# Kernel optimization log

Measured on AMD Instinct MI355X. Metric: run time of the kernel, lower is better.

Reference implementation:

```python
import jax, jax.numpy as jnp
import numpy as np

FSIZE = 5
PAD = FSIZE // 2


def _conv(mosaick, filts):
    # mosaick [B,1,H,W], filts [f,f,K] -> responses [B,K,H,W].
    # Cross-correlation with edge-clamped boundary (Halide clamp semantics).
    x = jnp.pad(mosaick, ((0, 0), (0, 0), (PAD, PAD), (PAD, PAD)), mode='edge')
    k = jnp.transpose(filts, (2, 0, 1))[:, None, :, :]  # [K,1,f,f] OIHW
    return jax.lax.conv_general_dilated(
        x, k, window_strides=(1, 1), padding='VALID',
        dimension_numbers=('NCHW', 'OIHW', 'NCHW'))


def setup_inputs() -> dict:
    key = jax.random.key(0)
    k1, k2, k3 = jax.random.split(key, 3)
    B, H, W, K, f = 16, 512, 512, 8, FSIZE
    std = 1.0 / (f * f)  # matches normal_(0, 1/(fsize*fsize))
    return {
        'mosaick': jax.random.normal(k1, (B, 1, H, W), dtype=jnp.float32),
        'sel_filts': jax.random.normal(k2, (f, f, K), dtype=jnp.float32) * std,
        'green_filts': jax.random.normal(k3, (f, f, K), dtype=jnp.float32) * std,
    }


def reference(mosaick, sel_filts, green_filts):
    # Per-pixel soft filter selection over K candidate green-interpolation filters.
    sel = _conv(mosaick, sel_filts)      # [B,K,H,W] selection scores
    grn = _conv(mosaick, green_filts)    # [B,K,H,W] candidate green estimates
    w = jax.nn.softmax(sel, axis=1)      # softmax over filter bank
    interp = jnp.sum(w * grn, axis=1, keepdims=True)  # [B,1,H,W]
    # GRBG Bayer: green where row parity == col parity; copy known greens.
    H, W = mosaick.shape[-2], mosaick.shape[-1]
    yy = jnp.arange(H)[:, None]
    xx = jnp.arange(W)[None, :]
    is_green = (yy % 2) == (xx % 2)      # [H,W] bool
    # Output green channel only (module returns output[:, 1:2, ...]).
    return jnp.where(is_green, mosaick, interp)
```

## Files before the change

### kernel.cpp

```cpp
#include <hip/hip_runtime.h>


typedef float f32x16 __attribute__((ext_vector_type(16)));
typedef short s16x8  __attribute__((ext_vector_type(8)));

#define HH 512
#define WW 512
#define TW 64
#define TH 16
#define RS 80
#define NROW 20
#define NEL 72

__device__ __forceinline__ unsigned short bf16rne(float x) {
    unsigned u = __float_as_uint(x);
    u += 0x7fffu + ((u >> 16) & 1u);
    return (unsigned short)(u >> 16);
}
__device__ __forceinline__ int pk2(float hi, float lo) {
    return (int)((((unsigned)bf16rne(hi)) << 16) | (unsigned)bf16rne(lo));
}
__device__ __forceinline__ float hi16(int v) { return __uint_as_float(((unsigned)v) & 0xffff0000u); }
__device__ __forceinline__ float lo16(int v) { return __uint_as_float(((unsigned)v) << 16); }

__global__ void build_frags_kernel(const float* __restrict__ sf,
                                   const float* __restrict__ gf,
                                   short* __restrict__ ws)
{
    const int lane = threadIdx.x;
    const int mm   = lane & 31;
    const int h    = (lane >> 5) & 1;
    const int c    = mm >> 1;
    const bool tg  = mm & 1;
    const bool chok = mm < 16;
    const float* fb = tg ? gf : sf;

    s16x8 A[6];
#pragma unroll
    for (int f = 0; f < 6; ++f)
#pragma unroll
        for (int j = 0; j < 8; ++j) A[f][j] = 0;

#pragma unroll
    for (int j = 0; j < 8; ++j) {
        const int dx0 = j - 1;
        if (dx0 >= 0 && dx0 < 5 && chok) {
            A[0][j] = (short)bf16rne(fb[((h)     * 5 + dx0) * 8 + c]);
            A[1][j] = (short)bf16rne(fb[((2 + h) * 5 + dx0) * 8 + c]);
            if (h == 0)
                A[2][j] = (short)bf16rne(fb[(4 * 5 + dx0) * 8 + c]);
        }
        const int dx1 = j;
        if (dx1 < 5 && chok) {
            if (h == 1)
                A[3][j] = (short)bf16rne(fb[(0 * 5 + dx1) * 8 + c]);
            A[4][j] = (short)bf16rne(fb[((1 + h) * 5 + dx1) * 8 + c]);
            A[5][j] = (short)bf16rne(fb[((3 + h) * 5 + dx1) * 8 + c]);
        }
    }
    s16x8* dst = (s16x8*)(ws + lane * 48);
#pragma unroll
    for (int f = 0; f < 6; ++f) dst[f] = A[f];
}

__global__ __launch_bounds__(256) void demosaick_kernel(
    const float* __restrict__ mos,
    const short* __restrict__ frg,
    float* __restrict__ out)
{
    __shared__ alignas(16) unsigned short tileS[NROW * RS];

    const int tid   = threadIdx.x;
    const int bx    = blockIdx.x;
    const int by    = blockIdx.y;
    const int bimg  = blockIdx.z;
    const int tileX = bx * TW;
    const int tileY = by * TH;
    const float* img = mos + (size_t)bimg * HH * WW;

    const bool interior = (bx >= 1) && (bx <= 6) && (by >= 1) && (by <= 30);
    if (interior) {
        if (tid < 180) {
            int r = tid / 9, s = tid - 9 * r;
            const float2* src = (const float2*)(img + (size_t)(tileY - 2 + r) * WW
                                                + (tileX - 2 + 8 * s));
            float2 v0 = src[0], v1 = src[1], v2 = src[2], v3 = src[3];
            int4 d;
            d.x = pk2(v0.y, v0.x);
            d.y = pk2(v1.y, v1.x);
            d.z = pk2(v2.y, v2.x);
            d.w = pk2(v3.y, v3.x);
            *(int4*)&tileS[r * RS + 8 * s] = d;
        }
    } else {
        for (int i = tid; i < NROW * NEL; i += 256) {
            int r = i / NEL, e = i - NEL * r;
            int gy = min(max(tileY - 2 + r, 0), HH - 1);
            int gx = min(max(tileX - 2 + e, 0), WW - 1);
            tileS[r * RS + e] = bf16rne(img[(size_t)gy * WW + gx]);
        }
    }

    const int lane = tid & 63;
    const int w    = tid >> 6;
    const int n    = lane & 31;
    const int h    = lane >> 5;

    const s16x8* wsf = (const s16x8*)(frg + lane * 48);
    const s16x8 Aa0 = wsf[0], Ab0 = wsf[1], Ac0 = wsf[2];
    const s16x8 Aa1 = wsf[3], Ab1 = wsf[4], Ac1 = wsf[5];

    __syncthreads();

    const int* tb = (const int*)tileS;
    float* outp = out + (size_t)bimg * HH * WW;

#pragma unroll
    for (int pp = 0; pp < 2; ++pp) {
        const int Rl = 4 * w + 2 * pp;
        const int y  = tileY + Rl;
        const int ia = (Rl + h) * 40 + n;

        union { int4 v; s16x8 s; } Ba, Bb, Bc;
        Ba.v.x = tb[ia];       Ba.v.y = tb[ia + 1];
        Ba.v.z = tb[ia + 2];   Ba.v.w = tb[ia + 3];
        Bb.v.x = tb[ia + 80];  Bb.v.y = tb[ia + 81];
        Bb.v.z = tb[ia + 82];  Bb.v.w = tb[ia + 83];
        Bc.v.x = tb[ia + 160]; Bc.v.y = tb[ia + 161];
        Bc.v.z = tb[ia + 162]; Bc.v.w = tb[ia + 163];

        f32x16 acc = (f32x16)(0.f);
        acc = __builtin_amdgcn_mfma_f32_32x32x16_bf16(Aa0, Ba.s, acc, 0, 0, 0);
        acc = __builtin_amdgcn_mfma_f32_32x32x16_bf16(Ab0, Bb.s, acc, 0, 0, 0);
        acc = __builtin_amdgcn_mfma_f32_32x32x16_bf16(Ac0, Bc.s, acc, 0, 0, 0);
        {
            float den = 0.f, num = 0.f;
#pragma unroll
            for (int j = 0; j < 4; ++j) {
                float e = __expf(acc[2 * j]);
                den += e;
                num = fmaf(e, acc[2 * j + 1], num);
            }
            int nd  = pk2(num, den);
            int nd2 = __shfl_xor(nd, 32);
            num += hi16(nd2);
            den += lo16(nd2);
            const float interp = num * __builtin_amdgcn_rcpf(den);
            if (h == 0) {
                const int x0 = tileX + 2 * n;
                const float green = img[(size_t)y * WW + x0];
                float2 st; st.x = green; st.y = interp;
                *(float2*)(outp + (size_t)y * WW + x0) = st;
            }
        }

        f32x16 acc2 = (f32x16)(0.f);
        acc2 = __builtin_amdgcn_mfma_f32_32x32x16_bf16(Aa1, Ba.s, acc2, 0, 0, 0);
        acc2 = __builtin_amdgcn_mfma_f32_32x32x16_bf16(Ab1, Bb.s, acc2, 0, 0, 0);
        acc2 = __builtin_amdgcn_mfma_f32_32x32x16_bf16(Ac1, Bc.s, acc2, 0, 0, 0);
        {
            float den = 0.f, num = 0.f;
#pragma unroll
            for (int j = 0; j < 4; ++j) {
                float e = __expf(acc2[2 * j]);
                den += e;
                num = fmaf(e, acc2[2 * j + 1], num);
            }
            int nd  = pk2(num, den);
            int nd2 = __shfl_xor(nd, 32);
            num += hi16(nd2);
            den += lo16(nd2);
            const float interp = num * __builtin_amdgcn_rcpf(den);
            if (h == 0) {
                const int x0 = tileX + 2 * n;
                const float green = img[(size_t)(y + 1) * WW + x0 + 1];
                float2 st; st.x = interp; st.y = green;
                *(float2*)(outp + (size_t)(y + 1) * WW + x0) = st;
            }
        }
    }
}

extern "C" void kernel_launch(void* const* d_in, const int* in_sizes, int n_in,
                              void* d_out, int out_size, void* d_ws, size_t ws_size,
                              hipStream_t stream) {
    const float* mos = (const float*)d_in[0];
    const float* sf  = (const float*)d_in[1];
    const float* gf  = (const float*)d_in[2];
    float* out = (float*)d_out;
    short* ws  = (short*)d_ws;

    const int B = in_sizes[0] / (HH * WW);

    build_frags_kernel<<<1, 64, 0, stream>>>(sf, gf, ws);

    dim3 grid(WW / TW, HH / TH, B);
    dim3 block(256);
    demosaick_kernel<<<grid, block, 0, stream>>>(mos, (const short*)ws, out);
}
```

Measured before the change: 85.73 us.

## Fuse fragment build into main kernel and merge even/odd MFMA passes

Removes the separate fragment-building launch, so each block now builds its bf16 filter fragments directly from the filter arrays in registers. The A-matrix layout is reorganised so a single 3-MFMA chain produces both even- and odd-row results (rows 0-15 and 16-31 of the output tile), halving MFMA count per row pair. B fragments for four tile rows are loaded once and shared across the two passes. The edge-clamp path is unified into the vectorised loader with a per-chunk clamped fallback. In exchange, every block redoes the filter gathers and bf16 conversion.

Result: no change. 84.45 us (-1.5%).

```diff
diff --git a/kernel.cpp b/kernel.cpp
--- a/kernel.cpp
+++ b/kernel.cpp
@@ -10,7 +10,6 @@
 #define TH 16
 #define RS 80
 #define NROW 20
-#define NEL 72
 
 __device__ __forceinline__ unsigned short bf16rne(float x) {
     unsigned u = __float_as_uint(x);
@@ -23,160 +22,123 @@
 __device__ __forceinline__ float hi16(int v) { return __uint_as_float(((unsigned)v) & 0xffff0000u); }
 __device__ __forceinline__ float lo16(int v) { return __uint_as_float(((unsigned)v) << 16); }
 
-__global__ void build_frags_kernel(const float* __restrict__ sf,
-                                   const float* __restrict__ gf,
-                                   short* __restrict__ ws)
-{
-    const int lane = threadIdx.x;
-    const int mm   = lane & 31;
-    const int h    = (lane >> 5) & 1;
-    const int c    = mm >> 1;
-    const bool tg  = mm & 1;
-    const bool chok = mm < 16;
-    const float* fb = tg ? gf : sf;
-
-    s16x8 A[6];
-#pragma unroll
-    for (int f = 0; f < 6; ++f)
-#pragma unroll
-        for (int j = 0; j < 8; ++j) A[f][j] = 0;
-
-#pragma unroll
-    for (int j = 0; j < 8; ++j) {
-        const int dx0 = j - 1;
-        if (dx0 >= 0 && dx0 < 5 && chok) {
-            A[0][j] = (short)bf16rne(fb[((h)     * 5 + dx0) * 8 + c]);
-            A[1][j] = (short)bf16rne(fb[((2 + h) * 5 + dx0) * 8 + c]);
-            if (h == 0)
-                A[2][j] = (short)bf16rne(fb[(4 * 5 + dx0) * 8 + c]);
-        }
-        const int dx1 = j;
-        if (dx1 < 5 && chok) {
-            if (h == 1)
-                A[3][j] = (short)bf16rne(fb[(0 * 5 + dx1) * 8 + c]);
-            A[4][j] = (short)bf16rne(fb[((1 + h) * 5 + dx1) * 8 + c]);
-            A[5][j] = (short)bf16rne(fb[((3 + h) * 5 + dx1) * 8 + c]);
-        }
-    }
-    s16x8* dst = (s16x8*)(ws + lane * 48);
-#pragma unroll
-    for (int f = 0; f < 6; ++f) dst[f] = A[f];
-}
-
 __global__ __launch_bounds__(256) void demosaick_kernel(
     const float* __restrict__ mos,
-    const short* __restrict__ frg,
+    const float* __restrict__ sf,
+    const float* __restrict__ gf,
     float* __restrict__ out)
 {
     __shared__ alignas(16) unsigned short tileS[NROW * RS];
 
     const int tid   = threadIdx.x;
-    const int bx    = blockIdx.x;
-    const int by    = blockIdx.y;
-    const int bimg  = blockIdx.z;
-    const int tileX = bx * TW;
-    const int tileY = by * TH;
-    const float* img = mos + (size_t)bimg * HH * WW;
+    const int tileX = blockIdx.x * TW;
+    const int tileY = blockIdx.y * TH;
+    const float* img = mos + (size_t)blockIdx.z * HH * WW;
 
-    const bool interior = (bx >= 1) && (bx <= 6) && (by >= 1) && (by <= 30);
-    if (interior) {
-        if (tid < 180) {
-            int r = tid / 9, s = tid - 9 * r;
-            const float2* src = (const float2*)(img + (size_t)(tileY - 2 + r) * WW
-                                                + (tileX - 2 + 8 * s));
+    if (tid < 180) {
+        int r = tid / 9, s = tid - 9 * r;
+        int gy = min(max(tileY - 2 + r, 0), HH - 1);
+        const float* rowp = img + (size_t)gy * WW;
+        int cx = tileX - 2 + 8 * s;
+        int4 d;
+        if (cx >= 0 && cx + 8 <= WW) {
+            const float2* src = (const float2*)(rowp + cx);
             float2 v0 = src[0], v1 = src[1], v2 = src[2], v3 = src[3];
-            int4 d;
             d.x = pk2(v0.y, v0.x);
             d.y = pk2(v1.y, v1.x);
             d.z = pk2(v2.y, v2.x);
             d.w = pk2(v3.y, v3.x);
-            *(int4*)&tileS[r * RS + 8 * s] = d;
+        } else {
+            float v[8];
+#pragma unroll
+            for (int j = 0; j < 8; ++j)
+                v[j] = rowp[min(max(cx + j, 0), WW - 1)];
+            d.x = pk2(v[1], v[0]);
+            d.y = pk2(v[3], v[2]);
+            d.z = pk2(v[5], v[4]);
+            d.w = pk2(v[7], v[6]);
         }
-    } else {
-        for (int i = tid; i < NROW * NEL; i += 256) {
-            int r = i / NEL, e = i - NEL * r;
-            int gy = min(max(tileY - 2 + r, 0), HH - 1);
-            int gx = min(max(tileX - 2 + e, 0), WW - 1);
-            tileS[r * RS + e] = bf16rne(img[(size_t)gy * WW + gx]);
+        *(int4*)&tileS[r * RS + 8 * s] = d;
+    }
+
+    const int lane = tid & 63;
+    const int m    = lane & 31;
+    const int h    = lane >> 5;
+    const int mc   = m & 15;
+    const int c    = mc >> 1;
+    const float* fb = (mc & 1) ? gf : sf;
+
+    s16x8 A0 = {0, 0, 0, 0, 0, 0, 0, 0}, A1 = A0, A2 = A0;
+#pragma unroll
+    for (int j = 0; j < 8; ++j) {
+        if (m < 16) {
+            int dx = j - 1;
+            if (dx >= 0 && dx < 5) {
+                A0[j] = (short)bf16rne(fb[(h * 5 + dx) * 8 + c]);
+                A1[j] = (short)bf16rne(fb[((2 + h) * 5 + dx) * 8 + c]);
+                if (h == 0)
+                    A2[j] = (short)bf16rne(fb[(20 + dx) * 8 + c]);
+            }
+        } else {
+            if (j < 5) {
+                if (h == 1)
+                    A0[j] = (short)bf16rne(fb[j * 8 + c]);
+                A1[j] = (short)bf16rne(fb[((1 + h) * 5 + j) * 8 + c]);
+                A2[j] = (short)bf16rne(fb[((3 + h) * 5 + j) * 8 + c]);
+            }
         }
     }
 
-    const int lane = tid & 63;
-    const int w    = tid >> 6;
-    const int n    = lane & 31;
-    const int h    = lane >> 5;
-
-    const s16x8* wsf = (const s16x8*)(frg + lane * 48);
-    const s16x8 Aa0 = wsf[0], Ab0 = wsf[1], Ac0 = wsf[2];
-    const s16x8 Aa1 = wsf[3], Ab1 = wsf[4], Ac1 = wsf[5];
-
     __syncthreads();
 
+    const int w = tid >> 6;
+    const int n = lane & 31;
     const int* tb = (const int*)tileS;
-    float* outp = out + (size_t)bimg * HH * WW;
+    float* outp = out + (size_t)blockIdx.z * HH * WW;
+
+    union { int4 v; s16x8 s; } F0, F1, F2, F3;
+    {
+        const int i0 = (4 * w + h) * 40 + n;
+        F0.v.x = tb[i0];       F0.v.y = tb[i0 + 1];   F0.v.z = tb[i0 + 2];   F0.v.w = tb[i0 + 3];
+        F1.v.x = tb[i0 + 80];  F1.v.y = tb[i0 + 81];  F1.v.z = tb[i0 + 82];  F1.v.w = tb[i0 + 83];
+        F2.v.x = tb[i0 + 160]; F2.v.y = tb[i0 + 161]; F2.v.z = tb[i0 + 162]; F2.v.w = tb[i0 + 163];
+        F3.v.x = tb[i0 + 240]; F3.v.y = tb[i0 + 241]; F3.v.z = tb[i0 + 242]; F3.v.w = tb[i0 + 243];
+    }
 
 #pragma unroll
     for (int pp = 0; pp < 2; ++pp) {
-        const int Rl = 4 * w + 2 * pp;
-        const int y  = tileY + Rl;
-        const int ia = (Rl + h) * 40 + n;
-
-        union { int4 v; s16x8 s; } Ba, Bb, Bc;
-        Ba.v.x = tb[ia];       Ba.v.y = tb[ia + 1];
-        Ba.v.z = tb[ia + 2];   Ba.v.w = tb[ia + 3];
-        Bb.v.x = tb[ia + 80];  Bb.v.y = tb[ia + 81];
-        Bb.v.z = tb[ia + 82];  Bb.v.w = tb[ia + 83];
-        Bc.v.x = tb[ia + 160]; Bc.v.y = tb[ia + 161];
-        Bc.v.z = tb[ia + 162]; Bc.v.w = tb[ia + 163];
+        const s16x8 Ba = (pp == 0) ? F0.s : F1.s;
+        const s16x8 Bb = (pp == 0) ? F1.s : F2.s;
+        const s16x8 Bc = (pp == 0) ? F2.s : F3.s;
 
         f32x16 acc = (f32x16)(0.f);
-        acc = __builtin_amdgcn_mfma_f32_32x32x16_bf16(Aa0, Ba.s, acc, 0, 0, 0);
-        acc = __builtin_amdgcn_mfma_f32_32x32x16_bf16(Ab0, Bb.s, acc, 0, 0, 0);
-        acc = __builtin_amdgcn_mfma_f32_32x32x16_bf16(Ac0, Bc.s, acc, 0, 0, 0);
-        {
-            float den = 0.f, num = 0.f;
+        acc = __builtin_amdgcn_mfma_f32_32x32x16_bf16(A0, Ba, acc, 0, 0, 0);
+        acc = __builtin_amdgcn_mfma_f32_32x32x16_bf16(A1, Bb, acc, 0, 0, 0);
+        acc = __builtin_amdgcn_mfma_f32_32x32x16_bf16(A2, Bc, acc, 0, 0, 0);
+
+        float denE = 0.f, numE = 0.f, denO = 0.f, numO = 0.f;
 #pragma unroll
-            for (int j = 0; j < 4; ++j) {
-                float e = __expf(acc[2 * j]);
-                den += e;
-                num = fmaf(e, acc[2 * j + 1], num);
-            }
-            int nd  = pk2(num, den);
-            int nd2 = __shfl_xor(nd, 32);
-            num += hi16(nd2);
-            den += lo16(nd2);
-            const float interp = num * __builtin_amdgcn_rcpf(den);
-            if (h == 0) {
-                const int x0 = tileX + 2 * n;
-                const float green = img[(size_t)y * WW + x0];
-                float2 st; st.x = green; st.y = interp;
-                *(float2*)(outp + (size_t)y * WW + x0) = st;
-            }
+        for (int j = 0; j < 4; ++j) {
+            float e  = __expf(acc[2 * j]);
+            denE += e;  numE = fmaf(e,  acc[2 * j + 1], numE);
+            float eo = __expf(acc[8 + 2 * j]);
+            denO += eo; numO = fmaf(eo, acc[9 + 2 * j], numO);
         }
+        int ndE  = pk2(numE, denE), ndO = pk2(numO, denO);
+        int ndE2 = __shfl_xor(ndE, 32);
+        int ndO2 = __shfl_xor(ndO, 32);
+        numE += hi16(ndE2); denE += lo16(ndE2);
+        numO += hi16(ndO2); denO += lo16(ndO2);
+        const float interpE = numE * __builtin_amdgcn_rcpf(denE);
+        const float interpO = numO * __builtin_amdgcn_rcpf(denO);
 
-        f32x16 acc2 = (f32x16)(0.f);
-        acc2 = __builtin_amdgcn_mfma_f32_32x32x16_bf16(Aa1, Ba.s, acc2, 0, 0, 0);
-        acc2 = __builtin_amdgcn_mfma_f32_32x32x16_bf16(Ab1, Bb.s, acc2, 0, 0, 0);
-        acc2 = __builtin_amdgcn_mfma_f32_32x32x16_bf16(Ac1, Bc.s, acc2, 0, 0, 0);
-        {
-            float den = 0.f, num = 0.f;
-#pragma unroll
-            for (int j = 0; j < 4; ++j) {
-                float e = __expf(acc2[2 * j]);
-                den += e;
-                num = fmaf(e, acc2[2 * j + 1], num);
-            }
-            int nd  = pk2(num, den);
-            int nd2 = __shfl_xor(nd, 32);
-            num += hi16(nd2);
-            den += lo16(nd2);
-            const float interp = num * __builtin_amdgcn_rcpf(den);
-            if (h == 0) {
-                const int x0 = tileX + 2 * n;
-                const float green = img[(size_t)(y + 1) * WW + x0 + 1];
-                float2 st; st.x = interp; st.y = green;
-                *(float2*)(outp + (size_t)(y + 1) * WW + x0) = st;
-            }
+        if (h == 0) {
+            const int x0 = tileX + 2 * n;
+            const int yE = tileY + 4 * w + 2 * pp;
+            float2 stE; stE.x = img[(size_t)yE * WW + x0]; stE.y = interpE;
+            *(float2*)(outp + (size_t)yE * WW + x0) = stE;
+            float2 stO; stO.x = interpO; stO.y = img[(size_t)(yE + 1) * WW + x0 + 1];
+            *(float2*)(outp + (size_t)(yE + 1) * WW + x0) = stO;
         }
     }
 }
@@ -188,13 +150,10 @@
     const float* sf  = (const float*)d_in[1];
     const float* gf  = (const float*)d_in[2];
     float* out = (float*)d_out;
-    short* ws  = (short*)d_ws;
 
-    const int B = in_sizes[0] / (HH * WW);
-
-    build_frags_kernel<<<1, 64, 0, stream>>>(sf, gf, ws);
-
-    dim3 grid(WW / TW, HH / TH, B);
+    const int B = in_sizes[0] / (HH * WW * 4) > 0 ? in_sizes[0] / (HH * WW) : 16;
+    dim3 grid(WW / TW, HH / TH, in_sizes[0] / (HH * WW));
     dim3 block(256);
-    demosaick_kernel<<<grid, block, 0, stream>>>(mos, (const short*)ws, out);
+    demosaick_kernel<<<grid, block, 0, stream>>>(mos, sf, gf, out);
+    (void)B; (void)d_ws; (void)ws_size; (void)n_in; (void)out_size;
 }
```
